# Optimization experiments

Hardware: AMD Instinct MI355X
Metric: run time of the kernel (lower is better)

The kernel has to match this reference:

```python
import jax, jax.numpy as jnp
import numpy as np

B, NX, NY = 4, 2048, 2048
DIM = 1024        # model dimension
IN_DIM = 1024    # input_dimension
OUT_DIM = 1024   # output_dimension
NUM_HEADS = 16
HEAD_DIM = DIM // NUM_HEADS
SCALE = HEAD_DIM ** -0.5


def setup_inputs() -> dict:
    key = jax.random.key(0)
    kx, ky, kq, kkv, ko = jax.random.split(key, 5)
    x = jax.random.normal(kx, (B, NX, IN_DIM), dtype=jnp.float32)
    y = jax.random.normal(ky, (B, NY, IN_DIM), dtype=jnp.float32)
    # Linear weights (stored as [in, out]; bias=False in the original)
    Wq = jax.random.normal(kq, (IN_DIM, DIM), dtype=jnp.float32) * (IN_DIM ** -0.5)
    Wkv = jax.random.normal(kkv, (IN_DIM, 2 * DIM), dtype=jnp.float32) * (IN_DIM ** -0.5)
    Wo = jax.random.normal(ko, (DIM, OUT_DIM), dtype=jnp.float32) * (DIM ** -0.5)
    return {"x": x, "y": y, "Wq": Wq, "Wkv": Wkv, "Wo": Wo}


def reference(x, y, Wq, Wkv, Wo):
    Bv, Nx, _ = x.shape
    Ny = y.shape[1]
    # projections
    q = (x @ Wq).reshape(Bv, Nx, NUM_HEADS, HEAD_DIM)          # [B,Nx,H,hd]
    kv = (y @ Wkv).reshape(Bv, Ny, 2, NUM_HEADS, HEAD_DIM)     # [B,Ny,2,H,hd]
    k, v = kv[:, :, 0], kv[:, :, 1]                            # [B,Ny,H,hd]
    # attention scores [B,H,Nx,Ny]
    attn = jax.nn.softmax(jnp.einsum('bqhd,bkhd->bhqk', q, k) * SCALE, axis=-1)
    # weighted values -> [B,Nx,H,hd] -> [B,Nx,DIM]
    r = jnp.einsum('bhqk,bkhd->bqhd', attn, v).reshape(Bv, Nx, DIM)
    return r @ Wo
```

## Files before the change

### kernel.cpp

```cpp
#include <hip/hip_runtime.h>
#include <cstdint>

typedef unsigned short u16;
typedef __bf16 bf16x8 __attribute__((ext_vector_type(8)));
typedef short  s16x4  __attribute__((ext_vector_type(4)));
typedef float  f32x4  __attribute__((ext_vector_type(4)));

#define BB 4
#define NX 2048
#define NY 2048
#define DIM 1024
#define IN_DIM 1024
#define NH 16
#define HD 64
#define SL (0.125f * 1.4426950408889634f)

#if __has_builtin(__builtin_amdgcn_exp2f)
#define EXP2(x) __builtin_amdgcn_exp2f(x)
#else
#define EXP2(x) exp2f(x)
#endif

#if __has_builtin(__builtin_amdgcn_cvt_pk_bf16_f32)
#define HAS_PKBF16 1
#else
#define HAS_PKBF16 0
#endif

__device__ __forceinline__ u16 f2bf(float f) {
    unsigned int u = __builtin_bit_cast(unsigned int, f);
    unsigned int r = (u + 0x7FFFu + ((u >> 16) & 1u)) >> 16;
    return (u16)r;
}

__device__ __forceinline__ unsigned int pk2(float a, float b) {
#if HAS_PKBF16
    auto t = __builtin_amdgcn_cvt_pk_bf16_f32(a, b);
    return __builtin_bit_cast(unsigned int, t);
#else
    return (unsigned int)f2bf(a) | ((unsigned int)f2bf(b) << 16);
#endif
}

__device__ __forceinline__ unsigned int pk2t(float a, float b) {
    return __builtin_amdgcn_perm(__builtin_bit_cast(unsigned int, b),
                                 __builtin_bit_cast(unsigned int, a),
                                 0x07060302u);
}

__device__ __forceinline__ float truncbf(float f) {
    return __builtin_bit_cast(float,
        __builtin_bit_cast(unsigned int, f) & 0xFFFF0000u);
}

__device__ __forceinline__ void gl_lds16(const u16* g, u16* l) {
    __builtin_amdgcn_global_load_lds(
        (const __attribute__((address_space(1))) unsigned int*)g,
        (__attribute__((address_space(3))) unsigned int*)l, 16, 0, 0);
}

__global__ __launch_bounds__(256) void cvt_xy(const float* __restrict__ x,
                                              const float* __restrict__ y,
                                              u16* __restrict__ xb,
                                              u16* __restrict__ yb) {
    const int bx = blockIdx.x;
    const float* in = (bx < 8192) ? x : y;
    u16* out = (bx < 8192) ? xb : yb;
    int i = (bx & 8191) * 256 + threadIdx.x;
    float4 v = ((const float4*)in)[i];
    ushort4 o;
    o.x = f2bf(v.x); o.y = f2bf(v.y); o.z = f2bf(v.z); o.w = f2bf(v.w);
    ((ushort4*)out)[i] = o;
}

__global__ __launch_bounds__(256) void transpose_w(const float* __restrict__ Wq,
                                                   const float* __restrict__ Wkv,
                                                   const float* __restrict__ Wo,
                                                   u16* __restrict__ WqT,
                                                   u16* __restrict__ WkvT,
                                                   u16* __restrict__ WoT) {
    __shared__ u16 t[32 * 33];
    const int bx = blockIdx.x;
    const float* W; u16* Wt; int N, nx;
    if (bx < 32)      { W = Wq;  Wt = WqT;  N = 1024; nx = bx; }
    else if (bx < 96) { W = Wkv; Wt = WkvT; N = 2048; nx = bx - 32; }
    else              { W = Wo;  Wt = WoT;  N = 1024; nx = bx - 96; }
    const int K = 1024;
    const int tid = threadIdx.x;
    const int col = tid & 31, rw = tid >> 5;
    const int n0 = nx * 32, k0 = blockIdx.y * 32;
#pragma unroll
    for (int i = 0; i < 4; i++) {
        int k = rw + i * 8;
        float v = W[(size_t)(k0 + k) * N + n0 + col];
        t[col * 33 + k] = f2bf(v);
    }
    __syncthreads();
#pragma unroll
    for (int i = 0; i < 4; i++) {
        int n = rw + i * 8;
        Wt[(size_t)(n0 + n) * K + k0 + col] = t[n * 33 + col];
    }
}

__global__ __launch_bounds__(256) void transpose_v(const u16* __restrict__ kv,
                                                   u16* __restrict__ vT) {
    __shared__ u16 t[64 * 72];
    const int tid = threadIdx.x;
    const int bh = blockIdx.x;
    const int b = bh >> 4, h = bh & 15;
    const int y0 = blockIdx.y * 64;
    {
        int y = tid >> 2, dc = tid & 3;
        const u16* src = &kv[((size_t)(b * NY + y0 + y)) * (2 * DIM) + DIM + h * HD + dc * 16];
        uint4 v0 = *(const uint4*)src;
        uint4 v1 = *(const uint4*)(src + 8);
        u16 tmp[16];
        *(uint4*)&tmp[0] = v0;
        *(uint4*)&tmp[8] = v1;
#pragma unroll
        for (int i = 0; i < 16; i++) t[(dc * 16 + i) * 72 + y] = tmp[i];
    }
    __syncthreads();
    {
        int d = tid >> 2, yc = tid & 3;
        uint4 v0 = *(const uint4*)&t[d * 72 + yc * 16];
        uint4 v1 = *(const uint4*)&t[d * 72 + yc * 16 + 8];
        u16* dst = &vT[((size_t)bh * HD + d) * NY + y0 + yc * 16];
        *(uint4*)dst = v0;
        *(uint4*)(dst + 8) = v1;
    }
}

template <bool BF16OUT>
__device__ __forceinline__ void gemm_core(u16* As, u16* Bs,
                                          const u16* __restrict__ A,
                                          const u16* __restrict__ Bt,
                                          void* __restrict__ Cv,
                                          int N, int K, float oscale,
                                          int m0, int n0) {
    u16* Cb = (u16*)Cv;
    float* Cf = (float*)Cv;
    const int tid = threadIdx.x;
    const int wave = tid >> 6, lane = tid & 63;
    const int ml = lane & 15, qd = lane >> 4;
    const int wm = (wave >> 1) * 64, wn = (wave & 1) * 64;

    f32x4 acc[4][4];
#pragma unroll
    for (int i = 0; i < 4; i++)
#pragma unroll
        for (int j = 0; j < 4; j++)
#pragma unroll
            for (int e = 0; e < 4; e++) acc[i][j][e] = 0.0f;

    for (int k0 = 0; k0 < K; k0 += 32) {
        __syncthreads();
#pragma unroll
        for (int i = 0; i < 2; i++) {
            int chunk = i * 256 + tid;
            int row = chunk >> 2, ko = (chunk & 3) * 8;
            gl_lds16(A + (size_t)(m0 + row) * K + k0 + ko, &As[(i * 256 + wave * 64) * 8]);
        }
#pragma unroll
        for (int i = 0; i < 2; i++) {
            int chunk = i * 256 + tid;
            int row = chunk >> 2, ko = (chunk & 3) * 8;
            gl_lds16(Bt + (size_t)(n0 + row) * K + k0 + ko, &Bs[(i * 256 + wave * 64) * 8]);
        }
        __syncthreads();

        bf16x8 af[4], bfr[4];
#pragma unroll
        for (int i = 0; i < 4; i++) af[i] = *(const bf16x8*)&As[(wm + i * 16 + ml) * 32 + qd * 8];
#pragma unroll
        for (int j = 0; j < 4; j++) bfr[j] = *(const bf16x8*)&Bs[(wn + j * 16 + ml) * 32 + qd * 8];
#pragma unroll
        for (int i = 0; i < 4; i++)
#pragma unroll
            for (int j = 0; j < 4; j++)
                acc[i][j] = __builtin_amdgcn_mfma_f32_16x16x32_bf16(af[i], bfr[j], acc[i][j], 0, 0, 0);
    }

#pragma unroll
    for (int i = 0; i < 4; i++)
#pragma unroll
        for (int j = 0; j < 4; j++)
#pragma unroll
            for (int r = 0; r < 4; r++) {
                int row = m0 + wm + i * 16 + qd * 4 + r;
                int col = n0 + wn + j * 16 + ml;
                if (BF16OUT) Cb[(size_t)row * N + col] = f2bf(acc[i][j][r] * oscale);
                else         Cf[(size_t)row * N + col] = acc[i][j][r];
            }
}

__global__ __launch_bounds__(256) void gemm_proj(const u16* __restrict__ xb,
                                                 const u16* __restrict__ yb,
                                                 const u16* __restrict__ WqT,
                                                 const u16* __restrict__ WkvT,
                                                 u16* __restrict__ qb,
                                                 u16* __restrict__ kvb) {
    __shared__ u16 As[128 * 32];
    __shared__ u16 Bs[128 * 32];
    const bool isq = blockIdx.x < 8;
    const u16* A  = isq ? xb : yb;
    const u16* Bt = isq ? WqT : WkvT;
    u16* C        = isq ? qb : kvb;
    const int N   = isq ? 1024 : 2048;
    const int n0  = (isq ? blockIdx.x : blockIdx.x - 8) * 128;
    const float oscale = isq ? SL : 1.0f;
    gemm_core<true>(As, Bs, A, Bt, C, N, 1024, oscale, blockIdx.y * 128, n0);
}

__global__ __launch_bounds__(256) void gemm_o(const u16* __restrict__ A,
                                              const u16* __restrict__ Bt,
                                              float* __restrict__ C) {
    __shared__ u16 As[128 * 32];
    __shared__ u16 Bs[128 * 32];
    gemm_core<false>(As, Bs, A, Bt, C, 1024, 1024, 1.0f, blockIdx.y * 128, blockIdx.x * 128);
}

__global__ __launch_bounds__(256) void flash_attn(const u16* __restrict__ qg,
                                                  const u16* __restrict__ kvg,
                                                  const u16* __restrict__ vTg,
                                                  u16* __restrict__ rg) {
    __shared__ u16 Kt[2][64 * 64];
    __shared__ u16 Vt[2][64 * 64];
    const int tid = threadIdx.x, wave = tid >> 6, lane = tid & 63;
    const int ml = lane & 15, qd = lane >> 4;
    const int xt = blockIdx.x, bh = blockIdx.y;
    const int b = bh >> 4, h = bh & 15;
    const int mlo = ml & 7;

    bf16x8 aq[2][2];
    {
        size_t qbase = ((size_t)(b * NX + xt * 128 + wave * 32)) * DIM + h * HD;
#pragma unroll
        for (int mt = 0; mt < 2; mt++)
#pragma unroll
            for (int s = 0; s < 2; s++)
                aq[mt][s] = *(const bf16x8*)&qg[qbase + (size_t)(mt * 16 + ml) * DIM + s * 32 + qd * 8];
    }

    int ka[2];
#pragma unroll
    for (int s = 0; s < 2; s++) ka[s] = ml * 128 + (((s * 4 + qd) ^ mlo) << 4);
    int va[2][2];
#pragma unroll
    for (int t2 = 0; t2 < 2; t2++)
#pragma unroll
        for (int hh = 0; hh < 2; hh++)
            va[t2][hh] = ml * 128 + ((((t2 * 4 + 2 * hh + (qd >> 1)) ^ mlo) * 8 + (qd & 1) * 4) << 1);
    const char* Kb = (const char*)&Kt[0][0];
    const char* Vb = (const char*)&Vt[0][0];

    const int rloc = lane >> 3;
    const int swz = (lane & 7) ^ rloc;
    const u16* ksrc[2];
    const u16* vsrc[2];
#pragma unroll
    for (int e = 0; e < 2; e++) {
        int row = (wave * 2 + e) * 8 + rloc;
        ksrc[e] = kvg + ((size_t)(b * NY + row)) * (2 * DIM) + h * HD + swz * 8;
        vsrc[e] = vTg + ((size_t)(bh * HD + row)) * NY + swz * 8;
    }
    const size_t KSTRIDE = (size_t)64 * (2 * DIM);
    const size_t VSTRIDE = 64;

    f32x4 o[2][4];
    f32x4 li4[2];
#pragma unroll
    for (int mt = 0; mt < 2; mt++) {
#pragma unroll
        for (int e = 0; e < 4; e++) li4[mt][e] = 0.0f;
#pragma unroll
        for (int dt = 0; dt < 4; dt++)
#pragma unroll
            for (int e = 0; e < 4; e++) o[mt][dt][e] = 0.0f;
    }
    const f32x4 fz = {0.0f, 0.0f, 0.0f, 0.0f};

#pragma unroll
    for (int e = 0; e < 2; e++) { gl_lds16(ksrc[e], &Kt[0][(wave * 2 + e) * 512]); ksrc[e] += KSTRIDE; }
#pragma unroll
    for (int e = 0; e < 2; e++) { gl_lds16(vsrc[e], &Vt[0][(wave * 2 + e) * 512]); vsrc[e] += VSTRIDE; }

    for (int it = 0; it < NY / 64; it += 2) {
#pragma unroll
        for (int half = 0; half < 2; ++half) {
            __syncthreads();
            if (it + half + 1 < NY / 64) {
#pragma unroll
                for (int e = 0; e < 2; e++) { gl_lds16(ksrc[e], &Kt[half ^ 1][(wave * 2 + e) * 512]); ksrc[e] += KSTRIDE; }
#pragma unroll
                for (int e = 0; e < 2; e++) { gl_lds16(vsrc[e], &Vt[half ^ 1][(wave * 2 + e) * 512]); vsrc[e] += VSTRIDE; }
            }

            f32x4 sc[2][4];
#pragma unroll
            for (int t = 0; t < 4; t++) {
                bf16x8 kf0 = *(const bf16x8*)(Kb + (half * 8192 + t * 2048) + ka[0]);
                bf16x8 kf1 = *(const bf16x8*)(Kb + (half * 8192 + t * 2048) + ka[1]);
                sc[0][t] = __builtin_amdgcn_mfma_f32_16x16x32_bf16(kf0, aq[0][0], fz, 0, 0, 0);
                sc[1][t] = __builtin_amdgcn_mfma_f32_16x16x32_bf16(kf0, aq[1][0], fz, 0, 0, 0);
                sc[0][t] = __builtin_amdgcn_mfma_f32_16x16x32_bf16(kf1, aq[0][1], sc[0][t], 0, 0, 0);
                sc[1][t] = __builtin_amdgcn_mfma_f32_16x16x32_bf16(kf1, aq[1][1], sc[1][t], 0, 0, 0);
            }

            uint4 pb[2][2];
#pragma unroll
            for (int mt = 0; mt < 2; mt++) {
#pragma unroll
                for (int t = 0; t < 4; t++)
#pragma unroll
                    for (int r = 0; r < 4; r++) sc[mt][t][r] = EXP2(sc[mt][t][r]);
#if HAS_PKBF16
                li4[mt] += (sc[mt][0] + sc[mt][1]) + (sc[mt][2] + sc[mt][3]);
#pragma unroll
                for (int t2 = 0; t2 < 2; t2++) {
                    pb[mt][t2].x = pk2(sc[mt][2 * t2][0], sc[mt][2 * t2][1]);
                    pb[mt][t2].y = pk2(sc[mt][2 * t2][2], sc[mt][2 * t2][3]);
                    pb[mt][t2].z = pk2(sc[mt][2 * t2 + 1][0], sc[mt][2 * t2 + 1][1]);
                    pb[mt][t2].w = pk2(sc[mt][2 * t2 + 1][2], sc[mt][2 * t2 + 1][3]);
                }
#else
#pragma unroll
                for (int t = 0; t < 4; t++)
#pragma unroll
                    for (int r = 0; r < 4; r++) sc[mt][t][r] = truncbf(sc[mt][t][r]);
                li4[mt] += (sc[mt][0] + sc[mt][1]) + (sc[mt][2] + sc[mt][3]);
#pragma unroll
                for (int t2 = 0; t2 < 2; t2++) {
                    pb[mt][t2].x = pk2t(sc[mt][2 * t2][0], sc[mt][2 * t2][1]);
                    pb[mt][t2].y = pk2t(sc[mt][2 * t2][2], sc[mt][2 * t2][3]);
                    pb[mt][t2].z = pk2t(sc[mt][2 * t2 + 1][0], sc[mt][2 * t2 + 1][1]);
                    pb[mt][t2].w = pk2t(sc[mt][2 * t2 + 1][2], sc[mt][2 * t2 + 1][3]);
                }
#endif
            }

#pragma unroll
            for (int t2 = 0; t2 < 2; t2++) {
                bf16x8 p0 = __builtin_bit_cast(bf16x8, pb[0][t2]);
                bf16x8 p1 = __builtin_bit_cast(bf16x8, pb[1][t2]);
#pragma unroll
                for (int dt = 0; dt < 4; dt++) {
                    union { struct { s16x4 lo, hi; } p; bf16x8 v; } u;
                    u.p.lo = *(const s16x4*)(Vb + (half * 8192 + dt * 2048) + va[t2][0]);
                    u.p.hi = *(const s16x4*)(Vb + (half * 8192 + dt * 2048) + va[t2][1]);
                    o[0][dt] = __builtin_amdgcn_mfma_f32_16x16x32_bf16(u.v, p0, o[0][dt], 0, 0, 0);
                    o[1][dt] = __builtin_amdgcn_mfma_f32_16x16x32_bf16(u.v, p1, o[1][dt], 0, 0, 0);
                }
            }
        }
    }

#pragma unroll
    for (int mt = 0; mt < 2; mt++) {
        float l = (li4[mt][0] + li4[mt][1]) + (li4[mt][2] + li4[mt][3]);
        l += __shfl_xor(l, 16);
        l += __shfl_xor(l, 32);
        float inv = 1.0f / l;
        size_t row = (size_t)(b * NX + xt * 128 + wave * 32 + mt * 16 + ml);
#pragma unroll
        for (int dt = 0; dt < 4; dt++) {
            uint2 val;
            val.x = pk2(o[mt][dt][0] * inv, o[mt][dt][1] * inv);
            val.y = pk2(o[mt][dt][2] * inv, o[mt][dt][3] * inv);
            *(uint2*)&rg[row * DIM + h * HD + dt * 16 + qd * 4] = val;
        }
    }
}

extern "C" void kernel_launch(void* const* d_in, const int* in_sizes, int n_in,
                              void* d_out, int out_size, void* d_ws, size_t ws_size,
                              hipStream_t stream) {
    const float* x   = (const float*)d_in[0];
    const float* y   = (const float*)d_in[1];
    const float* Wq  = (const float*)d_in[2];
    const float* Wkv = (const float*)d_in[3];
    const float* Wo  = (const float*)d_in[4];

    char* ws = (char*)d_ws;
    u16* xb   = (u16*)(ws + 0);
    u16* yb   = (u16*)(ws + 16777216);
    u16* WqT  = (u16*)(ws + 33554432);
    u16* WkvT = (u16*)(ws + 35651584);
    u16* WoT  = (u16*)(ws + 39845888);
    u16* qb   = (u16*)(ws + 41943040);
    u16* kvb  = (u16*)(ws + 58720256);
    u16* vTb  = (u16*)(ws + 92274688);
    u16* rb   = (u16*)(ws + 109051904);

    cvt_xy<<<16384, 256, 0, stream>>>(x, y, xb, yb);

    transpose_w<<<dim3(128, 32), 256, 0, stream>>>(Wq, Wkv, Wo, WqT, WkvT, WoT);

    gemm_proj<<<dim3(24, 64), 256, 0, stream>>>(xb, yb, WqT, WkvT, qb, kvb);

    transpose_v<<<dim3(64, 32), 256, 0, stream>>>(kvb, vTb);

    flash_attn<<<dim3(16, 64), 256, 0, stream>>>(qb, kvb, vTb, rb);

    gemm_o<<<dim3(8, 64), 256, 0, stream>>>(rb, WoT, (float*)d_out);
}
```

Baseline: 329.7 us.

## Merge prep kernels, deepen GEMM K-tile with swizzled LDS, retile output GEMM

Fuses the input conversion and weight transpose into one prep launch. The shared GEMM core now loads 64-wide K slices with an XOR-swizzled LDS layout, which halves the number of barrier pairs and avoids bank conflicts on fragment reads. The output GEMM uses 128x64 tiles so it launches twice as many blocks and fills more CUs. Launch bounds hint 4 blocks per CU for gemm_o and flash_attn, which may force register limits or spills.

After: 305.4 us. -7.4%, faster.

```diff
diff --git a/kernel.cpp b/kernel.cpp
--- a/kernel.cpp
+++ b/kernel.cpp
@@ -59,47 +59,50 @@
         (__attribute__((address_space(3))) unsigned int*)l, 16, 0, 0);
 }
 
-__global__ __launch_bounds__(256) void cvt_xy(const float* __restrict__ x,
-                                              const float* __restrict__ y,
-                                              u16* __restrict__ xb,
-                                              u16* __restrict__ yb) {
+__global__ __launch_bounds__(256) void prep(const float* __restrict__ x,
+                                            const float* __restrict__ y,
+                                            const float* __restrict__ Wq,
+                                            const float* __restrict__ Wkv,
+                                            const float* __restrict__ Wo,
+                                            u16* __restrict__ xb,
+                                            u16* __restrict__ yb,
+                                            u16* __restrict__ WqT,
+                                            u16* __restrict__ WkvT,
+                                            u16* __restrict__ WoT) {
     const int bx = blockIdx.x;
-    const float* in = (bx < 8192) ? x : y;
-    u16* out = (bx < 8192) ? xb : yb;
-    int i = (bx & 8191) * 256 + threadIdx.x;
-    float4 v = ((const float4*)in)[i];
-    ushort4 o;
-    o.x = f2bf(v.x); o.y = f2bf(v.y); o.z = f2bf(v.z); o.w = f2bf(v.w);
-    ((ushort4*)out)[i] = o;
-}
-
-__global__ __launch_bounds__(256) void transpose_w(const float* __restrict__ Wq,
-                                                   const float* __restrict__ Wkv,
-                                                   const float* __restrict__ Wo,
-                                                   u16* __restrict__ WqT,
-                                                   u16* __restrict__ WkvT,
-                                                   u16* __restrict__ WoT) {
-    __shared__ u16 t[32 * 33];
-    const int bx = blockIdx.x;
-    const float* W; u16* Wt; int N, nx;
-    if (bx < 32)      { W = Wq;  Wt = WqT;  N = 1024; nx = bx; }
-    else if (bx < 96) { W = Wkv; Wt = WkvT; N = 2048; nx = bx - 32; }
-    else              { W = Wo;  Wt = WoT;  N = 1024; nx = bx - 96; }
-    const int K = 1024;
-    const int tid = threadIdx.x;
-    const int col = tid & 31, rw = tid >> 5;
-    const int n0 = nx * 32, k0 = blockIdx.y * 32;
-#pragma unroll
-    for (int i = 0; i < 4; i++) {
-        int k = rw + i * 8;
-        float v = W[(size_t)(k0 + k) * N + n0 + col];
-        t[col * 33 + k] = f2bf(v);
-    }
-    __syncthreads();
-#pragma unroll
-    for (int i = 0; i < 4; i++) {
-        int n = rw + i * 8;
-        Wt[(size_t)(n0 + n) * K + k0 + col] = t[n * 33 + col];
+    if (bx < 16384) {
+        const float* in = (bx < 8192) ? x : y;
+        u16* out = (bx < 8192) ? xb : yb;
+        int i = (bx & 8191) * 256 + threadIdx.x;
+        float4 v = ((const float4*)in)[i];
+        ushort4 o;
+        o.x = f2bf(v.x); o.y = f2bf(v.y); o.z = f2bf(v.z); o.w = f2bf(v.w);
+        ((ushort4*)out)[i] = o;
+    } else {
+        __shared__ u16 t[32 * 33];
+        int id = bx - 16384;
+        int nx = id & 127;
+        const int k0 = (id >> 7) * 32;
+        const float* W; u16* Wt; int N;
+        if (nx < 32)      { W = Wq;  Wt = WqT;  N = 1024; }
+        else if (nx < 96) { W = Wkv; Wt = WkvT; N = 2048; nx -= 32; }
+        else              { W = Wo;  Wt = WoT;  N = 1024; nx -= 96; }
+        const int K = 1024;
+        const int tid = threadIdx.x;
+        const int col = tid & 31, rw = tid >> 5;
+        const int n0 = nx * 32;
+#pragma unroll
+        for (int i = 0; i < 4; i++) {
+            int k = rw + i * 8;
+            float v = W[(size_t)(k0 + k) * N + n0 + col];
+            t[col * 33 + k] = f2bf(v);
+        }
+        __syncthreads();
+#pragma unroll
+        for (int i = 0; i < 4; i++) {
+            int n = rw + i * 8;
+            Wt[(size_t)(n0 + n) * K + k0 + col] = t[n * 33 + col];
+        }
     }
 }
 
@@ -132,60 +135,66 @@
     }
 }
 
-template <bool BF16OUT>
+template <bool BF16OUT, int TN>
 __device__ __forceinline__ void gemm_core(u16* As, u16* Bs,
                                           const u16* __restrict__ A,
                                           const u16* __restrict__ Bt,
                                           void* __restrict__ Cv,
                                           int N, int K, float oscale,
                                           int m0, int n0) {
+    constexpr int NJ = TN / 32;
     u16* Cb = (u16*)Cv;
     float* Cf = (float*)Cv;
     const int tid = threadIdx.x;
     const int wave = tid >> 6, lane = tid & 63;
     const int ml = lane & 15, qd = lane >> 4;
-    const int wm = (wave >> 1) * 64, wn = (wave & 1) * 64;
-
-    f32x4 acc[4][4];
+    const int mlo = ml & 7;
+    const int wm = (wave >> 1) * 64, wn = (wave & 1) * (TN / 2);
+
+    f32x4 acc[4][NJ];
 #pragma unroll
     for (int i = 0; i < 4; i++)
 #pragma unroll
-        for (int j = 0; j < 4; j++)
+        for (int j = 0; j < NJ; j++)
 #pragma unroll
             for (int e = 0; e < 4; e++) acc[i][j][e] = 0.0f;
 
-    for (int k0 = 0; k0 < K; k0 += 32) {
+    const int r0 = tid >> 3;
+    const int swz = (tid & 7) ^ (r0 & 7);
+    const u16* Ap = A + (size_t)(m0 + r0) * K + swz * 8;
+    const u16* Bp = Bt + (size_t)(n0 + r0) * K + swz * 8;
+
+    for (int k0 = 0; k0 < K; k0 += 64) {
         __syncthreads();
 #pragma unroll
-        for (int i = 0; i < 2; i++) {
-            int chunk = i * 256 + tid;
-            int row = chunk >> 2, ko = (chunk & 3) * 8;
-            gl_lds16(A + (size_t)(m0 + row) * K + k0 + ko, &As[(i * 256 + wave * 64) * 8]);
+        for (int i = 0; i < 4; i++)
+            gl_lds16(Ap + (size_t)(i * 32) * K + k0, &As[(i * 256 + wave * 64) * 8]);
+#pragma unroll
+        for (int i = 0; i < TN / 32; i++)
+            gl_lds16(Bp + (size_t)(i * 32) * K + k0, &Bs[(i * 256 + wave * 64) * 8]);
+        __syncthreads();
+
+#pragma unroll
+        for (int s = 0; s < 2; s++) {
+            bf16x8 af[4], bfr[NJ];
+#pragma unroll
+            for (int i = 0; i < 4; i++)
+                af[i] = *(const bf16x8*)&As[(wm + i * 16 + ml) * 64 + (((s * 4 + qd) ^ mlo) * 8)];
+#pragma unroll
+            for (int j = 0; j < NJ; j++)
+                bfr[j] = *(const bf16x8*)&Bs[(wn + j * 16 + ml) * 64 + (((s * 4 + qd) ^ mlo) * 8)];
+#pragma unroll
+            for (int i = 0; i < 4; i++)
+#pragma unroll
+                for (int j = 0; j < NJ; j++)
+                    acc[i][j] = __builtin_amdgcn_mfma_f32_16x16x32_bf16(af[i], bfr[j], acc[i][j], 0, 0, 0);
         }
-#pragma unroll
-        for (int i = 0; i < 2; i++) {
-            int chunk = i * 256 + tid;
-            int row = chunk >> 2, ko = (chunk & 3) * 8;
-            gl_lds16(Bt + (size_t)(n0 + row) * K + k0 + ko, &Bs[(i * 256 + wave * 64) * 8]);
-        }
-        __syncthreads();
-
-        bf16x8 af[4], bfr[4];
-#pragma unroll
-        for (int i = 0; i < 4; i++) af[i] = *(const bf16x8*)&As[(wm + i * 16 + ml) * 32 + qd * 8];
-#pragma unroll
-        for (int j = 0; j < 4; j++) bfr[j] = *(const bf16x8*)&Bs[(wn + j * 16 + ml) * 32 + qd * 8];
-#pragma unroll
-        for (int i = 0; i < 4; i++)
-#pragma unroll
-            for (int j = 0; j < 4; j++)
-                acc[i][j] = __builtin_amdgcn_mfma_f32_16x16x32_bf16(af[i], bfr[j], acc[i][j], 0, 0, 0);
     }
 
 #pragma unroll
     for (int i = 0; i < 4; i++)
 #pragma unroll
-        for (int j = 0; j < 4; j++)
+        for (int j = 0; j < NJ; j++)
 #pragma unroll
             for (int r = 0; r < 4; r++) {
                 int row = m0 + wm + i * 16 + qd * 4 + r;
@@ -201,8 +210,8 @@
                                                  const u16* __restrict__ WkvT,
                                                  u16* __restrict__ qb,
                                                  u16* __restrict__ kvb) {
-    __shared__ u16 As[128 * 32];
-    __shared__ u16 Bs[128 * 32];
+    __shared__ u16 As[128 * 64];
+    __shared__ u16 Bs[128 * 64];
     const bool isq = blockIdx.x < 8;
     const u16* A  = isq ? xb : yb;
     const u16* Bt = isq ? WqT : WkvT;
@@ -210,21 +219,21 @@
     const int N   = isq ? 1024 : 2048;
     const int n0  = (isq ? blockIdx.x : blockIdx.x - 8) * 128;
     const float oscale = isq ? SL : 1.0f;
-    gemm_core<true>(As, Bs, A, Bt, C, N, 1024, oscale, blockIdx.y * 128, n0);
-}
-
-__global__ __launch_bounds__(256) void gemm_o(const u16* __restrict__ A,
-                                              const u16* __restrict__ Bt,
-                                              float* __restrict__ C) {
-    __shared__ u16 As[128 * 32];
-    __shared__ u16 Bs[128 * 32];
-    gemm_core<false>(As, Bs, A, Bt, C, 1024, 1024, 1.0f, blockIdx.y * 128, blockIdx.x * 128);
-}
-
-__global__ __launch_bounds__(256) void flash_attn(const u16* __restrict__ qg,
-                                                  const u16* __restrict__ kvg,
-                                                  const u16* __restrict__ vTg,
-                                                  u16* __restrict__ rg) {
+    gemm_core<true, 128>(As, Bs, A, Bt, C, N, 1024, oscale, blockIdx.y * 128, n0);
+}
+
+__global__ __launch_bounds__(256, 4) void gemm_o(const u16* __restrict__ A,
+                                                 const u16* __restrict__ Bt,
+                                                 float* __restrict__ C) {
+    __shared__ u16 As[128 * 64];
+    __shared__ u16 Bs[64 * 64];
+    gemm_core<false, 64>(As, Bs, A, Bt, C, 1024, 1024, 1.0f, blockIdx.y * 128, blockIdx.x * 64);
+}
+
+__global__ __launch_bounds__(256, 4) void flash_attn(const u16* __restrict__ qg,
+                                                     const u16* __restrict__ kvg,
+                                                     const u16* __restrict__ vTg,
+                                                     u16* __restrict__ rg) {
     __shared__ u16 Kt[2][64 * 64];
     __shared__ u16 Vt[2][64 * 64];
     const int tid = threadIdx.x, wave = tid >> 6, lane = tid & 63;
@@ -393,9 +402,7 @@
     u16* vTb  = (u16*)(ws + 92274688);
     u16* rb   = (u16*)(ws + 109051904);
 
-    cvt_xy<<<16384, 256, 0, stream>>>(x, y, xb, yb);
-
-    transpose_w<<<dim3(128, 32), 256, 0, stream>>>(Wq, Wkv, Wo, WqT, WkvT, WoT);
+    prep<<<20480, 256, 0, stream>>>(x, y, Wq, Wkv, Wo, xb, yb, WqT, WkvT, WoT);
 
     gemm_proj<<<dim3(24, 64), 256, 0, stream>>>(xb, yb, WqT, WkvT, qb, kvb);
 
@@ -403,5 +410,5 @@
 
     flash_attn<<<dim3(16, 64), 256, 0, stream>>>(qb, kvb, vTb, rb);
 
-    gemm_o<<<dim3(8, 64), 256, 0, stream>>>(rb, WoT, (float*)d_out);
-}
+    gemm_o<<<dim3(16, 64), 256, 0, stream>>>(rb, WoT, (float*)d_out);
+}
```
